# Kernel tuning notes

Measured on AMD Instinct MI355X. Metric: run time of the kernel, lower is better.

The kernel has to match this reference:

```python
import jax, jax.numpy as jnp
import numpy as np

N = 8192          # total nodes
G = 64            # graphs in batch
NPG = 128         # nodes per graph
K_NN = 100        # knn_graph k
F_IN = 6
WID = 128         # width
CONV_DEPTH = 3
LIN_DEPTH = 5
N_LAB = 1
D2 = 2 * CONV_DEPTH * WID  # 768
NEG_SLOPE = 0.01
BN_EPS = 1e-5


def setup_inputs() -> dict:
    key = jax.random.key(0)
    ks = jax.random.split(key, 12)
    s = 0.05
    return {
        "x": jax.random.normal(ks[0], (N, F_IN), jnp.float32),
        "batch": jnp.arange(N, dtype=jnp.int64) // NPG,  # 64 graphs x 128 nodes
        "conv1_W": jax.random.normal(ks[1], (F_IN, WID), jnp.float32) * s,
        "conv1_b": jnp.zeros((WID,), jnp.float32),
        "convs_W": jax.random.normal(ks[2], (CONV_DEPTH - 1, WID, WID), jnp.float32) * s,
        "convs_b": jnp.zeros((CONV_DEPTH - 1, WID), jnp.float32),
        "bn_gamma": jnp.ones((D2,), jnp.float32),
        "bn_beta": jnp.zeros((D2,), jnp.float32),
        "lin_W": jax.random.normal(ks[3], (LIN_DEPTH, D2, D2), jnp.float32) * s,
        "lin_b": jnp.zeros((LIN_DEPTH, D2), jnp.float32),
        "out_W": jax.random.normal(ks[4], (D2, N_LAB), jnp.float32) * s,
        "out_b": jnp.zeros((N_LAB,), jnp.float32),
    }


def _leaky(h):
    return jnp.where(h > 0, h, NEG_SLOPE * h)


def _knn_edges(x, batch):
    # squared pairwise distances, masked across graphs and on the diagonal
    sq = jnp.sum(x * x, axis=1)
    dist = sq[:, None] + sq[None, :] - 2.0 * (x @ x.T)          # [N, N]
    invalid = (batch[:, None] != batch[None, :]) | jnp.eye(N, dtype=bool)
    dist = jnp.where(invalid, jnp.inf, dist)
    # indices are non-differentiable; stop_gradient avoids keeping dist for bwd
    _, idx = jax.lax.top_k(-jax.lax.stop_gradient(dist), K_NN)   # [N, K_NN]
    row = idx.reshape(-1)                                        # sources (neighbors)
    col = jnp.repeat(jnp.arange(N), K_NN)                        # targets (centers)
    return row, col


def _sgconv(h, row, col, W, b):
    # SGConv, K=2: lin(((D^-1/2 (A+I) D^-1/2)^2) h)  -- gcn_norm w/ self loops
    loops = jnp.arange(N)
    rows = jnp.concatenate([row, loops])
    cols = jnp.concatenate([col, loops])
    deg = jax.ops.segment_sum(jnp.ones(rows.shape[0], h.dtype), cols, num_segments=N)
    dinv = jax.lax.rsqrt(deg)
    norm = dinv[rows] * dinv[cols]                               # [E]
    def prop(z):
        return jax.ops.segment_sum(norm[:, None] * z[rows], cols, num_segments=N)
    return prop(prop(h)) @ W + b


def _pool(h, batch):
    # concat(global_mean_pool, global_max_pool) -> [G, 2*width]
    counts = jax.ops.segment_sum(jnp.ones((N,), h.dtype), batch, num_segments=G)
    mean = jax.ops.segment_sum(h, batch, num_segments=G) / counts[:, None]
    mx = jax.ops.segment_max(h, batch, num_segments=G)
    return jnp.concatenate([mean, mx], axis=1)


def reference(x, batch, conv1_W, conv1_b, convs_W, convs_b,
              bn_gamma, bn_beta, lin_W, lin_b, out_W, out_b):
    batch = batch.astype(jnp.int32)
    row, col = _knn_edges(x, batch)
    # dropout_adj / Dropout are identity in eval mode
    h = _leaky(_sgconv(x, row, col, conv1_W, conv1_b))
    pools = [_pool(h, batch)]
    for f in range(CONV_DEPTH - 1):
        h = _leaky(_sgconv(h, row, col, convs_W[f], convs_b[f]))
        pools.append(_pool(h, batch))
    z = jnp.concatenate(pools, axis=1)                           # [G, 768]
    # BatchNorm1d (batch statistics, biased variance)
    m = jnp.mean(z, axis=0)
    v = jnp.mean((z - m) ** 2, axis=0)
    z = (z - m) * jax.lax.rsqrt(v + BN_EPS) * bn_gamma + bn_beta
    for g in range(LIN_DEPTH):
        z = _leaky(z @ lin_W[g] + lin_b[g])
    z = z @ out_W + out_b                                        # [G, 1]
    return z.reshape(-1)
```

## Files before the change

kernel.cpp:

```cpp
#include <hip/hip_runtime.h>

#define NN    8192
#define NG    64
#define NPG   128
#define KNN   100
#define FIN   6
#define WID   128
#define D2    768
#define NEG   0.01f
#define INV101 (1.0f/101.0f)
#define BNEPS 1e-5f
#define BIG   1e30f

__device__ __forceinline__ float leaky(float v) { return v > 0.f ? v : NEG * v; }

__global__ __launch_bounds__(256) void k_knn(const float* __restrict__ x, float* __restrict__ A)
{
    int g  = blockIdx.x >> 3;
    int i0 = (blockIdx.x & 7) * 16;
    __shared__ float xg[NPG * FIN];
    __shared__ float sq[NPG];
    __shared__ float D[16][NPG];
    const float* xp = x + g * NPG * FIN;
    for (int t = threadIdx.x; t < NPG * FIN; t += 256) xg[t] = xp[t];
    __syncthreads();
    if (threadIdx.x < NPG) {
        float s = 0.f;
        #pragma unroll
        for (int c = 0; c < FIN; ++c) { float v = xg[threadIdx.x * FIN + c]; s = fmaf(v, v, s); }
        sq[threadIdx.x] = s;
    }
    __syncthreads();
    for (int e = threadIdx.x; e < 16 * NPG; e += 256) {
        int il = e >> 7, j = e & 127;
        int i = i0 + il;
        float d;
        if (j == i) d = BIG;
        else {
            float dot = 0.f;
            #pragma unroll
            for (int c = 0; c < FIN; ++c) dot = fmaf(xg[i * FIN + c], xg[j * FIN + c], dot);
            d = sq[i] + sq[j] - 2.f * dot;
        }
        D[il][j] = d;
    }
    __syncthreads();
    float* Ag = A + (size_t)g * NPG * NPG;
    for (int e = threadIdx.x; e < 16 * NPG; e += 256) {
        int il = e >> 7, j = e & 127;
        int i = i0 + il;
        float aval;
        if (i == j) aval = INV101;
        else {
            float dj = D[il][j];
            int cnt = 0;
            #pragma unroll 8
            for (int k = 0; k < NPG; ++k) {
                float dk = D[il][k];
                cnt += (dk < dj || (dk == dj && k < j)) ? 1 : 0;
            }
            aval = (cnt < KNN) ? INV101 : 0.f;
        }
        Ag[i * NPG + j] = aval;
    }
}

__global__ __launch_bounds__(256) void k_sqA(const float* __restrict__ A, float* __restrict__ A2)
{
    int g = blockIdx.x >> 1;
    int i0 = (blockIdx.x & 1) * 64;
    __shared__ float As[64 * 129];
    __shared__ float Bs[NPG * 132];
    const float* Ag = A + (size_t)g * NPG * NPG;
    for (int t = threadIdx.x; t < NPG * NPG; t += 256) {
        int r = t >> 7, c = t & 127;
        Bs[r * 132 + c] = Ag[t];
    }
    for (int t = threadIdx.x; t < 64 * NPG; t += 256) {
        int r = t >> 7, c = t & 127;
        As[r * 129 + c] = Ag[(i0 + r) * NPG + c];
    }
    __syncthreads();
    int ty = threadIdx.x >> 4, tx = threadIdx.x & 15;
    int lr = ty * 4, cj = tx * 8;
    float acc[4][8] = {};
    for (int k = 0; k < NPG; ++k) {
        float a[4], bb[8];
        #pragma unroll
        for (int r = 0; r < 4; ++r) a[r] = As[(lr + r) * 129 + k];
        float4 b0 = *(const float4*)&Bs[k * 132 + cj];
        float4 b1 = *(const float4*)&Bs[k * 132 + cj + 4];
        bb[0]=b0.x; bb[1]=b0.y; bb[2]=b0.z; bb[3]=b0.w;
        bb[4]=b1.x; bb[5]=b1.y; bb[6]=b1.z; bb[7]=b1.w;
        #pragma unroll
        for (int r = 0; r < 4; ++r)
            #pragma unroll
            for (int c = 0; c < 8; ++c)
                acc[r][c] = fmaf(a[r], bb[c], acc[r][c]);
    }
    float* A2g = A2 + (size_t)g * NPG * NPG;
    #pragma unroll
    for (int r = 0; r < 4; ++r) {
        float4 v0 = {acc[r][0], acc[r][1], acc[r][2], acc[r][3]};
        float4 v1 = {acc[r][4], acc[r][5], acc[r][6], acc[r][7]};
        *(float4*)&A2g[(i0 + lr + r) * NPG + cj]     = v0;
        *(float4*)&A2g[(i0 + lr + r) * NPG + cj + 4] = v1;
    }
}

__global__ __launch_bounds__(256) void k_conv1(const float* __restrict__ x, const float* __restrict__ A2,
                                               const float* __restrict__ W1, const float* __restrict__ b1,
                                               float* __restrict__ H)
{
    int g = blockIdx.x;
    __shared__ float xg[NPG * FIN];
    __shared__ float p2[NPG * FIN];
    const float* xp = x + g * NPG * FIN;
    for (int t = threadIdx.x; t < NPG * FIN; t += 256) xg[t] = xp[t];
    __syncthreads();
    const float* A2g = A2 + (size_t)g * NPG * NPG;
    for (int e = threadIdx.x; e < NPG * FIN; e += 256) {
        int i = e / FIN, d = e - i * FIN;
        float s = 0.f;
        for (int k = 0; k < NPG; ++k) s = fmaf(A2g[i * NPG + k], xg[k * FIN + d], s);
        p2[e] = s;
    }
    __syncthreads();
    for (int e = threadIdx.x; e < NPG * WID; e += 256) {
        int i = e >> 7, o = e & 127;
        float s = b1[o];
        #pragma unroll
        for (int d = 0; d < FIN; ++d) s = fmaf(p2[i * FIN + d], W1[d * WID + o], s);
        H[(size_t)(g * NPG + i) * WID + o] = leaky(s);
    }
}

__global__ __launch_bounds__(256) void k_conv(const float* __restrict__ A2, const float* __restrict__ Hin,
                                              const float* __restrict__ W, const float* __restrict__ bias,
                                              float* __restrict__ Hout, float* __restrict__ Zp, int zoff)
{
    int g = blockIdx.x >> 1;
    int i0 = (blockIdx.x & 1) * 64;
    __shared__ float Ps[64 * 129];
    __shared__ float hs[NPG * 132];
    const float* A2g = A2 + (size_t)g * NPG * NPG + (size_t)i0 * NPG;
    const float* hg  = Hin + (size_t)g * NPG * WID;
    for (int t = threadIdx.x; t < NPG * WID; t += 256) {
        int r = t >> 7, c = t & 127;
        hs[r * 132 + c] = hg[t];
    }
    for (int t = threadIdx.x; t < 64 * NPG; t += 256) {
        int r = t >> 7, c = t & 127;
        Ps[r * 129 + c] = A2g[t];
    }
    __syncthreads();
    if (i0 == 0 && threadIdx.x < WID) {
        int o = threadIdx.x;
        float sm = 0.f, mx = -BIG;
        for (int i = 0; i < NPG; ++i) { float v = hs[i * 132 + o]; sm += v; mx = fmaxf(mx, v); }
        Zp[g * D2 + zoff + o]       = sm * (1.f / NPG);
        Zp[g * D2 + zoff + WID + o] = mx;
    }
    int ty = threadIdx.x >> 4, tx = threadIdx.x & 15;
    int lr = ty * 4, cj = tx * 8;
    {
        float acc[4][8] = {};
        for (int k = 0; k < NPG; ++k) {
            float a[4], bb[8];
            #pragma unroll
            for (int r = 0; r < 4; ++r) a[r] = Ps[(lr + r) * 129 + k];
            float4 b0 = *(const float4*)&hs[k * 132 + cj];
            float4 b1 = *(const float4*)&hs[k * 132 + cj + 4];
            bb[0]=b0.x; bb[1]=b0.y; bb[2]=b0.z; bb[3]=b0.w;
            bb[4]=b1.x; bb[5]=b1.y; bb[6]=b1.z; bb[7]=b1.w;
            #pragma unroll
            for (int r = 0; r < 4; ++r)
                #pragma unroll
                for (int c = 0; c < 8; ++c)
                    acc[r][c] = fmaf(a[r], bb[c], acc[r][c]);
        }
        __syncthreads();
        #pragma unroll
        for (int r = 0; r < 4; ++r)
            #pragma unroll
            for (int c = 0; c < 8; ++c)
                Ps[(lr + r) * 129 + cj + c] = acc[r][c];
        __syncthreads();
    }
    {
        float acc[4][8] = {};
        for (int d = 0; d < NPG; ++d) {
            float a[4], bb[8];
            #pragma unroll
            for (int r = 0; r < 4; ++r) a[r] = Ps[(lr + r) * 129 + d];
            float4 w0 = *(const float4*)&W[d * WID + cj];
            float4 w1 = *(const float4*)&W[d * WID + cj + 4];
            bb[0]=w0.x; bb[1]=w0.y; bb[2]=w0.z; bb[3]=w0.w;
            bb[4]=w1.x; bb[5]=w1.y; bb[6]=w1.z; bb[7]=w1.w;
            #pragma unroll
            for (int r = 0; r < 4; ++r)
                #pragma unroll
                for (int c = 0; c < 8; ++c)
                    acc[r][c] = fmaf(a[r], bb[c], acc[r][c]);
        }
        #pragma unroll
        for (int r = 0; r < 4; ++r) {
            float4 v0, v1;
            v0.x = leaky(acc[r][0] + bias[cj + 0]);
            v0.y = leaky(acc[r][1] + bias[cj + 1]);
            v0.z = leaky(acc[r][2] + bias[cj + 2]);
            v0.w = leaky(acc[r][3] + bias[cj + 3]);
            v1.x = leaky(acc[r][4] + bias[cj + 4]);
            v1.y = leaky(acc[r][5] + bias[cj + 5]);
            v1.z = leaky(acc[r][6] + bias[cj + 6]);
            v1.w = leaky(acc[r][7] + bias[cj + 7]);
            *(float4*)&Hout[(size_t)(g * NPG + i0 + lr + r) * WID + cj]     = v0;
            *(float4*)&Hout[(size_t)(g * NPG + i0 + lr + r) * WID + cj + 4] = v1;
        }
    }
}

__global__ __launch_bounds__(128) void k_pool(const float* __restrict__ H, float* __restrict__ Zp, int zoff)
{
    int g = blockIdx.x, o = threadIdx.x;
    float sm = 0.f, mx = -BIG;
    for (int i = 0; i < NPG; ++i) {
        float v = H[((size_t)g * NPG + i) * WID + o];
        sm += v; mx = fmaxf(mx, v);
    }
    Zp[g * D2 + zoff + o]       = sm * (1.f / NPG);
    Zp[g * D2 + zoff + WID + o] = mx;
}

__global__ __launch_bounds__(128) void k_bn(const float* __restrict__ Zp, const float* __restrict__ gam,
                                            const float* __restrict__ bet, float* __restrict__ ZT)
{
    int c = blockIdx.x * 128 + threadIdx.x;
    float s = 0.f, s2 = 0.f;
    for (int r = 0; r < NG; ++r) { float v = Zp[r * D2 + c]; s += v; s2 = fmaf(v, v, s2); }
    float m   = s * (1.f / NG);
    float var = s2 * (1.f / NG) - m * m;
    float sc  = rsqrtf(var + BNEPS) * gam[c];
    float bt  = bet[c];
    for (int r = 0; r < NG; ++r) {
        float v = Zp[r * D2 + c];
        ZT[c * NG + r] = (v - m) * sc + bt;
    }
}

__global__ __launch_bounds__(256) void k_linA(const float* __restrict__ ZTin, const float* __restrict__ W,
                                              float* __restrict__ P)
{
    const int c  = blockIdx.x * 16 + (threadIdx.x & 15);
    const int r0 = (threadIdx.x >> 4) * 4;
    const int k0 = blockIdx.y * 96;
    const float* wp = W + (size_t)k0 * D2 + c;
    const float* zp = ZTin + k0 * NG + r0;
    float4 acc = {0.f, 0.f, 0.f, 0.f};
    for (int kk = 0; kk < 96; kk += 16) {
        float  wv[16];
        float4 zv[16];
        #pragma unroll
        for (int u = 0; u < 16; ++u) {
            wv[u] = wp[(kk + u) * D2];
            zv[u] = *(const float4*)&zp[(kk + u) * NG];
        }
        #pragma unroll
        for (int u = 0; u < 16; ++u) {
            acc.x = fmaf(zv[u].x, wv[u], acc.x);
            acc.y = fmaf(zv[u].y, wv[u], acc.y);
            acc.z = fmaf(zv[u].z, wv[u], acc.z);
            acc.w = fmaf(zv[u].w, wv[u], acc.w);
        }
    }
    *(float4*)&P[((size_t)blockIdx.y * D2 + c) * NG + r0] = acc;
}

__global__ __launch_bounds__(256) void k_linB(const float* __restrict__ P, const float* __restrict__ bias,
                                              float* __restrict__ ZTout)
{
    int e = (blockIdx.x * 256 + threadIdx.x) * 4;
    float4 s = *(const float4*)&P[e];
    #pragma unroll
    for (int q = 1; q < 8; ++q) {
        float4 p = *(const float4*)&P[(size_t)q * (D2 * NG) + e];
        s.x += p.x; s.y += p.y; s.z += p.z; s.w += p.w;
    }
    float bv = bias[e >> 6];
    s.x = leaky(s.x + bv); s.y = leaky(s.y + bv);
    s.z = leaky(s.z + bv); s.w = leaky(s.w + bv);
    *(float4*)&ZTout[e] = s;
}

__global__ __launch_bounds__(256) void k_out(const float* __restrict__ ZTin, const float* __restrict__ W,
                                             const float* __restrict__ bias, float* __restrict__ out)
{
    __shared__ float red[4][64];
    int r = threadIdx.x & 63, q = threadIdx.x >> 6;
    float s = 0.f;
    #pragma unroll 8
    for (int k = q * 192; k < q * 192 + 192; ++k)
        s = fmaf(ZTin[k * NG + r], W[k], s);
    red[q][r] = s;
    __syncthreads();
    if (threadIdx.x < 64)
        out[r] = red[0][r] + red[1][r] + red[2][r] + red[3][r] + bias[0];
}

extern "C" void kernel_launch(void* const* d_in, const int* in_sizes, int n_in,
                              void* d_out, int out_size, void* d_ws, size_t ws_size,
                              hipStream_t stream)
{
    (void)in_sizes; (void)n_in; (void)out_size; (void)ws_size;
    const float* x       = (const float*)d_in[0];
    const float* conv1_W = (const float*)d_in[2];
    const float* conv1_b = (const float*)d_in[3];
    const float* convs_W = (const float*)d_in[4];
    const float* convs_b = (const float*)d_in[5];
    const float* bn_g    = (const float*)d_in[6];
    const float* bn_b    = (const float*)d_in[7];
    const float* lin_W   = (const float*)d_in[8];
    const float* lin_b   = (const float*)d_in[9];
    const float* out_W   = (const float*)d_in[10];
    const float* out_b   = (const float*)d_in[11];

    float* A_raw = (float*)d_ws;
    float* A2    = A_raw + (1 << 20);
    float* H_a   = A2 + (1 << 20);
    float* H_b   = A_raw;
    float* P     = A_raw;
    float* Zp    = H_a + (1 << 20);
    float* ZT0   = Zp + NG * D2;
    float* ZT1   = ZT0 + NG * D2;

    k_knn  <<<dim3(512), dim3(256), 0, stream>>>(x, A_raw);
    k_sqA  <<<dim3(128), dim3(256), 0, stream>>>(A_raw, A2);
    k_conv1<<<dim3(NG),  dim3(256), 0, stream>>>(x, A2, conv1_W, conv1_b, H_a);
    k_conv <<<dim3(128), dim3(256), 0, stream>>>(A2, H_a, convs_W,             convs_b,       H_b, Zp, 0);
    k_conv <<<dim3(128), dim3(256), 0, stream>>>(A2, H_b, convs_W + WID * WID, convs_b + WID, H_a, Zp, 256);
    k_pool <<<dim3(NG),  dim3(128), 0, stream>>>(H_a, Zp, 512);
    k_bn   <<<dim3(6),   dim3(128), 0, stream>>>(Zp, bn_g, bn_b, ZT0);

    const float* zin = ZT0; float* zout = ZT1;
    for (int l = 0; l < 5; ++l) {
        k_linA<<<dim3(48, 8), dim3(256), 0, stream>>>(zin, lin_W + (size_t)l * D2 * D2, P);
        k_linB<<<dim3(48),    dim3(256), 0, stream>>>(P, lin_b + l * D2, zout);
        float* t = zout; zout = (float*)zin; zin = t;
    }
    k_out<<<dim3(1), dim3(256), 0, stream>>>(zin, out_W, out_b, (float*)d_out);
}
```

Before: 191.3 us.

## Fuse A-squaring with conv1, split conv blocks finer, deepen linA split-K

Merges the A² computation and the first SGConv projection into one kernel, so conv1 reads A² rows from shared memory instead of re-reading them from global memory, and one launch is removed. The A²/conv kernels now split each graph into four 32-row blocks (256 blocks instead of 128) with vectorized float4 staging and unpadded B tiles, trading more redundant loading of the full neighbour matrix per block for higher parallelism. The linear layers use a 16-way split-K instead of 8, which doubles partial-sum traffic in linB. Unpadded 128-stride shared tiles may cause bank conflicts.

```diff
diff --git a/kernel.cpp b/kernel.cpp
--- a/kernel.cpp
+++ b/kernel.cpp
@@ -65,73 +65,75 @@
     }
 }
 
-__global__ __launch_bounds__(256) void k_sqA(const float* __restrict__ A, float* __restrict__ A2)
-{
-    int g = blockIdx.x >> 1;
-    int i0 = (blockIdx.x & 1) * 64;
-    __shared__ float As[64 * 129];
-    __shared__ float Bs[NPG * 132];
+__global__ __launch_bounds__(256) void k_sqA_c1(const float* __restrict__ A, const float* __restrict__ x,
+                                                const float* __restrict__ W1, const float* __restrict__ b1,
+                                                float* __restrict__ A2, float* __restrict__ H)
+{
+    int g  = blockIdx.x >> 2;
+    int i0 = (blockIdx.x & 2) << 4;
+    i0 = (blockIdx.x & 3) * 32;
+    __shared__ float As[32 * 132];
+    __shared__ float Bs[NPG * NPG];
+    __shared__ float xg[NPG * FIN];
+    __shared__ float p2[32 * FIN];
+    __shared__ float W1s[FIN * WID];
+    __shared__ float b1s[WID];
     const float* Ag = A + (size_t)g * NPG * NPG;
-    for (int t = threadIdx.x; t < NPG * NPG; t += 256) {
-        int r = t >> 7, c = t & 127;
-        Bs[r * 132 + c] = Ag[t];
-    }
-    for (int t = threadIdx.x; t < 64 * NPG; t += 256) {
-        int r = t >> 7, c = t & 127;
-        As[r * 129 + c] = Ag[(i0 + r) * NPG + c];
-    }
-    __syncthreads();
+    const float* xp = x + g * NPG * FIN;
+    for (int t4 = threadIdx.x; t4 < NPG * NPG / 4; t4 += 256)
+        *(float4*)&Bs[t4 * 4] = *(const float4*)&Ag[t4 * 4];
+    for (int t4 = threadIdx.x; t4 < 32 * 32; t4 += 256) {
+        int r = t4 >> 5, c4 = (t4 & 31) * 4;
+        *(float4*)&As[r * 132 + c4] = *(const float4*)&Ag[(i0 + r) * NPG + c4];
+    }
+    for (int t = threadIdx.x; t < NPG * FIN; t += 256) xg[t] = xp[t];
+    for (int t = threadIdx.x; t < FIN * WID; t += 256) W1s[t] = W1[t];
+    if (threadIdx.x < WID) b1s[threadIdx.x] = b1[threadIdx.x];
+    __syncthreads();
+
     int ty = threadIdx.x >> 4, tx = threadIdx.x & 15;
-    int lr = ty * 4, cj = tx * 8;
-    float acc[4][8] = {};
+    int r0 = ty * 2, cj = tx * 8;
+    float acc[2][8] = {};
     for (int k = 0; k < NPG; ++k) {
-        float a[4], bb[8];
-        #pragma unroll
-        for (int r = 0; r < 4; ++r) a[r] = As[(lr + r) * 129 + k];
-        float4 b0 = *(const float4*)&Bs[k * 132 + cj];
-        float4 b1 = *(const float4*)&Bs[k * 132 + cj + 4];
-        bb[0]=b0.x; bb[1]=b0.y; bb[2]=b0.z; bb[3]=b0.w;
-        bb[4]=b1.x; bb[5]=b1.y; bb[6]=b1.z; bb[7]=b1.w;
-        #pragma unroll
-        for (int r = 0; r < 4; ++r)
-            #pragma unroll
-            for (int c = 0; c < 8; ++c)
-                acc[r][c] = fmaf(a[r], bb[c], acc[r][c]);
+        float a0 = As[r0 * 132 + k];
+        float a1 = As[(r0 + 1) * 132 + k];
+        float4 q0 = *(const float4*)&Bs[k * NPG + cj];
+        float4 q1 = *(const float4*)&Bs[k * NPG + cj + 4];
+        float bb[8] = {q0.x, q0.y, q0.z, q0.w, q1.x, q1.y, q1.z, q1.w};
+        #pragma unroll
+        for (int c = 0; c < 8; ++c) {
+            acc[0][c] = fmaf(a0, bb[c], acc[0][c]);
+            acc[1][c] = fmaf(a1, bb[c], acc[1][c]);
+        }
     }
     float* A2g = A2 + (size_t)g * NPG * NPG;
     #pragma unroll
-    for (int r = 0; r < 4; ++r) {
+    for (int r = 0; r < 2; ++r) {
         float4 v0 = {acc[r][0], acc[r][1], acc[r][2], acc[r][3]};
         float4 v1 = {acc[r][4], acc[r][5], acc[r][6], acc[r][7]};
-        *(float4*)&A2g[(i0 + lr + r) * NPG + cj]     = v0;
-        *(float4*)&A2g[(i0 + lr + r) * NPG + cj + 4] = v1;
-    }
-}
-
-__global__ __launch_bounds__(256) void k_conv1(const float* __restrict__ x, const float* __restrict__ A2,
-                                               const float* __restrict__ W1, const float* __restrict__ b1,
-                                               float* __restrict__ H)
-{
-    int g = blockIdx.x;
-    __shared__ float xg[NPG * FIN];
-    __shared__ float p2[NPG * FIN];
-    const float* xp = x + g * NPG * FIN;
-    for (int t = threadIdx.x; t < NPG * FIN; t += 256) xg[t] = xp[t];
-    __syncthreads();
-    const float* A2g = A2 + (size_t)g * NPG * NPG;
-    for (int e = threadIdx.x; e < NPG * FIN; e += 256) {
-        int i = e / FIN, d = e - i * FIN;
+        *(float4*)&A2g[(i0 + r0 + r) * NPG + cj]     = v0;
+        *(float4*)&A2g[(i0 + r0 + r) * NPG + cj + 4] = v1;
+    }
+    __syncthreads();
+    #pragma unroll
+    for (int r = 0; r < 2; ++r) {
+        *(float4*)&As[(r0 + r) * 132 + cj]     = make_float4(acc[r][0], acc[r][1], acc[r][2], acc[r][3]);
+        *(float4*)&As[(r0 + r) * 132 + cj + 4] = make_float4(acc[r][4], acc[r][5], acc[r][6], acc[r][7]);
+    }
+    __syncthreads();
+    if (threadIdx.x < 32 * FIN) {
+        int i = threadIdx.x / FIN, d = threadIdx.x - i * FIN;
         float s = 0.f;
-        for (int k = 0; k < NPG; ++k) s = fmaf(A2g[i * NPG + k], xg[k * FIN + d], s);
-        p2[e] = s;
-    }
-    __syncthreads();
-    for (int e = threadIdx.x; e < NPG * WID; e += 256) {
+        for (int k = 0; k < NPG; ++k) s = fmaf(As[i * 132 + k], xg[k * FIN + d], s);
+        p2[threadIdx.x] = s;
+    }
+    __syncthreads();
+    for (int e = threadIdx.x; e < 32 * WID; e += 256) {
         int i = e >> 7, o = e & 127;
-        float s = b1[o];
-        #pragma unroll
-        for (int d = 0; d < FIN; ++d) s = fmaf(p2[i * FIN + d], W1[d * WID + o], s);
-        H[(size_t)(g * NPG + i) * WID + o] = leaky(s);
+        float s = b1s[o];
+        #pragma unroll
+        for (int d = 0; d < FIN; ++d) s = fmaf(p2[i * FIN + d], W1s[d * WID + o], s);
+        H[(size_t)(g * NPG + i0 + i) * WID + o] = leaky(s);
     }
 }
 
@@ -139,83 +141,85 @@
                                               const float* __restrict__ W, const float* __restrict__ bias,
                                               float* __restrict__ Hout, float* __restrict__ Zp, int zoff)
 {
-    int g = blockIdx.x >> 1;
-    int i0 = (blockIdx.x & 1) * 64;
-    __shared__ float Ps[64 * 129];
-    __shared__ float hs[NPG * 132];
-    const float* A2g = A2 + (size_t)g * NPG * NPG + (size_t)i0 * NPG;
+    int g  = blockIdx.x >> 2;
+    int i0 = (blockIdx.x & 3) * 32;
+    __shared__ float Ps[32 * 132];
+    __shared__ float hs[NPG * WID];
+    const float* A2g = A2 + (size_t)g * NPG * NPG;
     const float* hg  = Hin + (size_t)g * NPG * WID;
-    for (int t = threadIdx.x; t < NPG * WID; t += 256) {
-        int r = t >> 7, c = t & 127;
-        hs[r * 132 + c] = hg[t];
-    }
-    for (int t = threadIdx.x; t < 64 * NPG; t += 256) {
-        int r = t >> 7, c = t & 127;
-        Ps[r * 129 + c] = A2g[t];
-    }
-    __syncthreads();
-    if (i0 == 0 && threadIdx.x < WID) {
+    for (int t4 = threadIdx.x; t4 < NPG * WID / 4; t4 += 256)
+        *(float4*)&hs[t4 * 4] = *(const float4*)&hg[t4 * 4];
+    for (int t4 = threadIdx.x; t4 < 32 * 32; t4 += 256) {
+        int r = t4 >> 5, c4 = (t4 & 31) * 4;
+        *(float4*)&Ps[r * 132 + c4] = *(const float4*)&A2g[(i0 + r) * NPG + c4];
+    }
+    __syncthreads();
+    if ((blockIdx.x & 3) == 0 && threadIdx.x < WID) {
         int o = threadIdx.x;
         float sm = 0.f, mx = -BIG;
-        for (int i = 0; i < NPG; ++i) { float v = hs[i * 132 + o]; sm += v; mx = fmaxf(mx, v); }
+        for (int i = 0; i < NPG; ++i) { float v = hs[i * WID + o]; sm += v; mx = fmaxf(mx, v); }
         Zp[g * D2 + zoff + o]       = sm * (1.f / NPG);
         Zp[g * D2 + zoff + WID + o] = mx;
     }
     int ty = threadIdx.x >> 4, tx = threadIdx.x & 15;
-    int lr = ty * 4, cj = tx * 8;
+    int r0 = ty * 2, cj = tx * 8;
+    float acc[2][8];
     {
-        float acc[4][8] = {};
+        #pragma unroll
+        for (int r = 0; r < 2; ++r)
+            #pragma unroll
+            for (int c = 0; c < 8; ++c) acc[r][c] = 0.f;
         for (int k = 0; k < NPG; ++k) {
-            float a[4], bb[8];
-            #pragma unroll
-            for (int r = 0; r < 4; ++r) a[r] = Ps[(lr + r) * 129 + k];
-            float4 b0 = *(const float4*)&hs[k * 132 + cj];
-            float4 b1 = *(const float4*)&hs[k * 132 + cj + 4];
-            bb[0]=b0.x; bb[1]=b0.y; bb[2]=b0.z; bb[3]=b0.w;
-            bb[4]=b1.x; bb[5]=b1.y; bb[6]=b1.z; bb[7]=b1.w;
-            #pragma unroll
-            for (int r = 0; r < 4; ++r)
-                #pragma unroll
-                for (int c = 0; c < 8; ++c)
-                    acc[r][c] = fmaf(a[r], bb[c], acc[r][c]);
+            float a0 = Ps[r0 * 132 + k];
+            float a1 = Ps[(r0 + 1) * 132 + k];
+            float4 q0 = *(const float4*)&hs[k * WID + cj];
+            float4 q1 = *(const float4*)&hs[k * WID + cj + 4];
+            float bb[8] = {q0.x, q0.y, q0.z, q0.w, q1.x, q1.y, q1.z, q1.w};
+            #pragma unroll
+            for (int c = 0; c < 8; ++c) {
+                acc[0][c] = fmaf(a0, bb[c], acc[0][c]);
+                acc[1][c] = fmaf(a1, bb[c], acc[1][c]);
+            }
         }
         __syncthreads();
         #pragma unroll
-        for (int r = 0; r < 4; ++r)
-            #pragma unroll
-            for (int c = 0; c < 8; ++c)
-                Ps[(lr + r) * 129 + cj + c] = acc[r][c];
+        for (int r = 0; r < 2; ++r) {
+            *(float4*)&Ps[(r0 + r) * 132 + cj]     = make_float4(acc[r][0], acc[r][1], acc[r][2], acc[r][3]);
+            *(float4*)&Ps[(r0 + r) * 132 + cj + 4] = make_float4(acc[r][4], acc[r][5], acc[r][6], acc[r][7]);
+        }
         __syncthreads();
     }
     {
-        float acc[4][8] = {};
+        float o2[2][8];
+        #pragma unroll
+        for (int r = 0; r < 2; ++r)
+            #pragma unroll
+            for (int c = 0; c < 8; ++c) o2[r][c] = 0.f;
         for (int d = 0; d < NPG; ++d) {
-            float a[4], bb[8];
-            #pragma unroll
-            for (int r = 0; r < 4; ++r) a[r] = Ps[(lr + r) * 129 + d];
+            float a0 = Ps[r0 * 132 + d];
+            float a1 = Ps[(r0 + 1) * 132 + d];
             float4 w0 = *(const float4*)&W[d * WID + cj];
             float4 w1 = *(const float4*)&W[d * WID + cj + 4];
-            bb[0]=w0.x; bb[1]=w0.y; bb[2]=w0.z; bb[3]=w0.w;
-            bb[4]=w1.x; bb[5]=w1.y; bb[6]=w1.z; bb[7]=w1.w;
-            #pragma unroll
-            for (int r = 0; r < 4; ++r)
-                #pragma unroll
-                for (int c = 0; c < 8; ++c)
-                    acc[r][c] = fmaf(a[r], bb[c], acc[r][c]);
-        }
-        #pragma unroll
-        for (int r = 0; r < 4; ++r) {
+            float bb[8] = {w0.x, w0.y, w0.z, w0.w, w1.x, w1.y, w1.z, w1.w};
+            #pragma unroll
+            for (int c = 0; c < 8; ++c) {
+                o2[0][c] = fmaf(a0, bb[c], o2[0][c]);
+                o2[1][c] = fmaf(a1, bb[c], o2[1][c]);
+            }
+        }
+        #pragma unroll
+        for (int r = 0; r < 2; ++r) {
             float4 v0, v1;
-            v0.x = leaky(acc[r][0] + bias[cj + 0]);
-            v0.y = leaky(acc[r][1] + bias[cj + 1]);
-            v0.z = leaky(acc[r][2] + bias[cj + 2]);
-            v0.w = leaky(acc[r][3] + bias[cj + 3]);
-            v1.x = leaky(acc[r][4] + bias[cj + 4]);
-            v1.y = leaky(acc[r][5] + bias[cj + 5]);
-            v1.z = leaky(acc[r][6] + bias[cj + 6]);
-            v1.w = leaky(acc[r][7] + bias[cj + 7]);
-            *(float4*)&Hout[(size_t)(g * NPG + i0 + lr + r) * WID + cj]     = v0;
-            *(float4*)&Hout[(size_t)(g * NPG + i0 + lr + r) * WID + cj + 4] = v1;
+            v0.x = leaky(o2[r][0] + bias[cj + 0]);
+            v0.y = leaky(o2[r][1] + bias[cj + 1]);
+            v0.z = leaky(o2[r][2] + bias[cj + 2]);
+            v0.w = leaky(o2[r][3] + bias[cj + 3]);
+            v1.x = leaky(o2[r][4] + bias[cj + 4]);
+            v1.y = leaky(o2[r][5] + bias[cj + 5]);
+            v1.z = leaky(o2[r][6] + bias[cj + 6]);
+            v1.w = leaky(o2[r][7] + bias[cj + 7]);
+            *(float4*)&Hout[(size_t)(g * NPG + i0 + r0 + r) * WID + cj]     = v0;
+            *(float4*)&Hout[(size_t)(g * NPG + i0 + r0 + r) * WID + cj + 4] = v1;
         }
     }
 }
@@ -253,11 +257,12 @@
 {
     const int c  = blockIdx.x * 16 + (threadIdx.x & 15);
     const int r0 = (threadIdx.x >> 4) * 4;
-    const int k0 = blockIdx.y * 96;
+    const int k0 = blockIdx.y * 48;
     const float* wp = W + (size_t)k0 * D2 + c;
     const float* zp = ZTin + k0 * NG + r0;
     float4 acc = {0.f, 0.f, 0.f, 0.f};
-    for (int kk = 0; kk < 96; kk += 16) {
+    #pragma unroll
+    for (int kk = 0; kk < 48; kk += 16) {
         float  wv[16];
         float4 zv[16];
         #pragma unroll
@@ -282,7 +287,7 @@
     int e = (blockIdx.x * 256 + threadIdx.x) * 4;
     float4 s = *(const float4*)&P[e];
     #pragma unroll
-    for (int q = 1; q < 8; ++q) {
+    for (int q = 1; q < 16; ++q) {
         float4 p = *(const float4*)&P[(size_t)q * (D2 * NG) + e];
         s.x += p.x; s.y += p.y; s.z += p.z; s.w += p.w;
     }
@@ -333,18 +338,17 @@
     float* ZT0   = Zp + NG * D2;
     float* ZT1   = ZT0 + NG * D2;
 
-    k_knn  <<<dim3(512), dim3(256), 0, stream>>>(x, A_raw);
-    k_sqA  <<<dim3(128), dim3(256), 0, stream>>>(A_raw, A2);
-    k_conv1<<<dim3(NG),  dim3(256), 0, stream>>>(x, A2, conv1_W, conv1_b, H_a);
-    k_conv <<<dim3(128), dim3(256), 0, stream>>>(A2, H_a, convs_W,             convs_b,       H_b, Zp, 0);
-    k_conv <<<dim3(128), dim3(256), 0, stream>>>(A2, H_b, convs_W + WID * WID, convs_b + WID, H_a, Zp, 256);
-    k_pool <<<dim3(NG),  dim3(128), 0, stream>>>(H_a, Zp, 512);
-    k_bn   <<<dim3(6),   dim3(128), 0, stream>>>(Zp, bn_g, bn_b, ZT0);
+    k_knn   <<<dim3(512), dim3(256), 0, stream>>>(x, A_raw);
+    k_sqA_c1<<<dim3(256), dim3(256), 0, stream>>>(A_raw, x, conv1_W, conv1_b, A2, H_a);
+    k_conv  <<<dim3(256), dim3(256), 0, stream>>>(A2, H_a, convs_W,             convs_b,       H_b, Zp, 0);
+    k_conv  <<<dim3(256), dim3(256), 0, stream>>>(A2, H_b, convs_W + WID * WID, convs_b + WID, H_a, Zp, 256);
+    k_pool  <<<dim3(NG),  dim3(128), 0, stream>>>(H_a, Zp, 512);
+    k_bn    <<<dim3(6),   dim3(128), 0, stream>>>(Zp, bn_g, bn_b, ZT0);
 
     const float* zin = ZT0; float* zout = ZT1;
     for (int l = 0; l < 5; ++l) {
-        k_linA<<<dim3(48, 8), dim3(256), 0, stream>>>(zin, lin_W + (size_t)l * D2 * D2, P);
-        k_linB<<<dim3(48),    dim3(256), 0, stream>>>(P, lin_b + l * D2, zout);
+        k_linA<<<dim3(48, 16), dim3(256), 0, stream>>>(zin, lin_W + (size_t)l * D2 * D2, P);
+        k_linB<<<dim3(48),     dim3(256), 0, stream>>>(P, lin_b + l * D2, zout);
         float* t = zout; zout = (float*)zin; zin = t;
     }
     k_out<<<dim3(1), dim3(256), 0, stream>>>(zin, out_W, out_b, (float*)d_out);
```

New measurement: 172.2 us. -10.0%, faster.
